# Optimization experiments

Measured on AMD Instinct MI355X. Metric: run time of the kernel, lower is better.

## Reference

```python
import jax, jax.numpy as jnp
import numpy as np

NUM_EMBEDDINGS = 512
EMBEDDING_DIM = 64
COMMITMENT_COST = 0.25
N_TOKENS = 262144


def setup_inputs() -> dict:
    key = jax.random.key(0)
    kz, kc = jax.random.split(key)
    z = jax.random.normal(kz, (N_TOKENS, EMBEDDING_DIM), dtype=jnp.float32)
    # nn.Embedding weight init: uniform(-1/num_embeddings, 1/num_embeddings)
    codebook = jax.random.uniform(
        kc, (NUM_EMBEDDINGS, EMBEDDING_DIM), dtype=jnp.float32,
        minval=-1.0 / NUM_EMBEDDINGS, maxval=1.0 / NUM_EMBEDDINGS)
    return {"z": z, "codebook": codebook}


def reference(z, codebook):
    # squared L2 distances: [N, K]
    distances = (jnp.sum(z * z, axis=1, keepdims=True)
                 + jnp.sum(codebook * codebook, axis=1)
                 - 2.0 * z @ codebook.T)
    encoding_indices = jnp.argmin(distances, axis=1)  # [N]
    z_q = codebook[encoding_indices]                  # [N, D] gather

    e_latent_loss = jnp.mean((jax.lax.stop_gradient(z_q) - z) ** 2)
    q_latent_loss = jnp.mean((z_q - jax.lax.stop_gradient(z)) ** 2)
    loss = q_latent_loss + COMMITMENT_COST * e_latent_loss

    # straight-through estimator
    z_q_st = z + jax.lax.stop_gradient(z_q - z)
    return (z_q_st, loss)
```

## Files before the change

kernel.cpp:

```cpp
#include <hip/hip_runtime.h>
#include <hip/hip_bf16.h>

#define N_TOKENS   262144
#define DIM        64
#define KCODES     512
#define OUT_ELEMS  (N_TOKENS * DIM)
#define LOSS_SCALE (1.25f / 16777216.0f)

typedef float  f32x4 __attribute__((ext_vector_type(4)));
typedef float  f32x8 __attribute__((ext_vector_type(8)));
typedef int    i32x4 __attribute__((ext_vector_type(4)));
typedef int    i32x2 __attribute__((ext_vector_type(2)));

static __device__ __forceinline__ long pack_fp8x8(const f32x8 v) {
    int lo = __builtin_amdgcn_cvt_pk_fp8_f32(v[0], v[1], 0, false);
    lo     = __builtin_amdgcn_cvt_pk_fp8_f32(v[2], v[3], lo, true);
    int hi = __builtin_amdgcn_cvt_pk_fp8_f32(v[4], v[5], 0, false);
    hi     = __builtin_amdgcn_cvt_pk_fp8_f32(v[6], v[7], hi, true);
    i32x2 r = {lo, hi};
    return __builtin_bit_cast(long, r);
}

__global__ void vq_prep(const float* __restrict__ cb,
                        unsigned char* __restrict__ cbf,
                        float* __restrict__ c2,
                        float* __restrict__ out_loss) {
    const int k = blockIdx.x;
    const int d = threadIdx.x;
    const float v = cb[k * DIM + d];
    float s = v * v;
    #pragma unroll
    for (int sh = 1; sh < 64; sh <<= 1) s += __shfl_xor(s, sh, 64);
    if (d == 0) c2[k] = 128.0f * s + 256.0f;

    const int t = k >> 4, li = k & 15;
    const int kk = d >> 5, hi = (d >> 3) & 3, j = d & 7;
    const int slot = (t * 2 + kk) * 64 + hi * 16 + li;
    const int p = __builtin_amdgcn_cvt_pk_fp8_f32(-256.0f * v, 0.0f, 0, false);
    cbf[slot * 8 + j] = (unsigned char)(p & 0xFF);

    if (k == 0 && d == 0) *out_loss = 0.0f;
}

__global__ __launch_bounds__(512, 4) void vq_main(
    const float* __restrict__ z,
    const float* __restrict__ cb,
    const unsigned char* __restrict__ cbf,
    const float* __restrict__ c2g,
    float* __restrict__ out)
{
    __shared__ unsigned char cbs[KCODES * DIM];
    __shared__ float c2s[KCODES];
    __shared__ int   keysl[8][32];
    __shared__ float lpart[8];

    const int tid  = threadIdx.x;
    const int wave = tid >> 6;
    const int lane = tid & 63;
    const int li   = lane & 15;
    const int hi   = lane >> 4;

    const int token0 = blockIdx.x * 256 + wave * 32;

    const float* zb = z + (size_t)token0 * DIM + li * DIM + hi * 8;
    const f32x8 v00 = *(const f32x8*)(zb);
    const f32x8 v01 = *(const f32x8*)(zb + 32);
    const f32x8 v10 = *(const f32x8*)(zb + 16 * DIM);
    const f32x8 v11 = *(const f32x8*)(zb + 16 * DIM + 32);

    #pragma unroll
    for (int i = 0; i < 4; ++i)
        ((i32x4*)cbs)[i * 512 + tid] = ((const i32x4*)cbf)[i * 512 + tid];
    c2s[tid] = c2g[tid];

    long af[2][2];
    float z2[2];
    {
        float zs = 0.f;
        #pragma unroll
        for (int j = 0; j < 8; ++j) zs += v00[j] * v00[j] + v01[j] * v01[j];
        af[0][0] = pack_fp8x8(v00);
        af[0][1] = pack_fp8x8(v01);
        zs += __shfl_xor(zs, 16, 64);
        zs += __shfl_xor(zs, 32, 64);
        z2[0] = zs;
    }
    {
        float zs = 0.f;
        #pragma unroll
        for (int j = 0; j < 8; ++j) zs += v10[j] * v10[j] + v11[j] * v11[j];
        af[1][0] = pack_fp8x8(v10);
        af[1][1] = pack_fp8x8(v11);
        zs += __shfl_xor(zs, 16, 64);
        zs += __shfl_xor(zs, 32, 64);
        z2[1] = zs;
    }
    __syncthreads();

    unsigned bkey[2][4];
    #pragma unroll
    for (int m = 0; m < 2; ++m)
        #pragma unroll
        for (int r = 0; r < 4; ++r) bkey[m][r] = 0xFFFFFFFFu;

    #pragma unroll 4
    for (int t = 0; t < 32; ++t) {
        const long b0 = *(const long*)&cbs[((t * 2 + 0) * 64 + lane) * 8];
        const long b1 = *(const long*)&cbs[((t * 2 + 1) * 64 + lane) * 8];
        const float cv = c2s[t * 16 + li];
        const unsigned code = (unsigned)(t * 16 + li);
        #pragma unroll
        for (int m = 0; m < 2; ++m) {
            f32x4 acc = {cv, cv, cv, cv};
            acc = __builtin_amdgcn_mfma_f32_16x16x32_fp8_fp8(af[m][0], b0, acc, 0, 0, 0);
            acc = __builtin_amdgcn_mfma_f32_16x16x32_fp8_fp8(af[m][1], b1, acc, 0, 0, 0);
            #pragma unroll
            for (int r = 0; r < 4; ++r) {
                const unsigned key = (__builtin_bit_cast(unsigned, acc[r]) & ~511u) | code;
                if (key < bkey[m][r]) bkey[m][r] = key;
            }
        }
    }

    #pragma unroll
    for (int sh = 1; sh < 16; sh <<= 1) {
        #pragma unroll
        for (int m = 0; m < 2; ++m)
            #pragma unroll
            for (int r = 0; r < 4; ++r) {
                const unsigned ok = (unsigned)__shfl_xor((int)bkey[m][r], sh, 64);
                if (ok < bkey[m][r]) bkey[m][r] = ok;
            }
    }

    if (li == 0) {
        #pragma unroll
        for (int m = 0; m < 2; ++m)
            #pragma unroll
            for (int r = 0; r < 4; ++r)
                keysl[wave][m * 16 + hi * 4 + r] = (int)bkey[m][r];
    }

    float lossp = 0.f;
    #pragma unroll
    for (int m = 0; m < 2; ++m) {
        const unsigned key = (unsigned)keysl[wave][m * 16 + li];
        const int code = (int)(key & 511u);
        if (hi == 0) {
            const float kf = __builtin_bit_cast(float, key & ~511u);
            lossp += __builtin_fmaf(kf - 256.0f, 0.0078125f, z2[m]);
        }
        const float* cbr = cb + code * DIM + hi * 8;
        const f32x8 q0 = *(const f32x8*)(cbr);
        const f32x8 q1 = *(const f32x8*)(cbr + 32);
        float* op = out + (size_t)(token0 + m * 16 + li) * DIM + hi * 8;
        *(f32x8*)(op)      = q0;
        *(f32x8*)(op + 32) = q1;
    }

    #pragma unroll
    for (int sh = 1; sh < 64; sh <<= 1) lossp += __shfl_xor(lossp, sh, 64);
    if (lane == 0) lpart[wave] = lossp;
    __syncthreads();
    if (tid == 0) {
        float s = 0.f;
        #pragma unroll
        for (int w = 0; w < 8; ++w) s += lpart[w];
        atomicAdd(out + OUT_ELEMS, s * LOSS_SCALE);
    }
}

extern "C" void kernel_launch(void* const* d_in, const int* in_sizes, int n_in,
                              void* d_out, int out_size, void* d_ws, size_t ws_size,
                              hipStream_t stream) {
    const float* z  = (const float*)d_in[0];
    const float* cb = (const float*)d_in[1];
    float* out = (float*)d_out;

    unsigned char* cbf = (unsigned char*)d_ws;
    float* c2 = (float*)((char*)d_ws + KCODES * DIM);

    vq_prep<<<KCODES, 64, 0, stream>>>(cb, cbf, c2, out + OUT_ELEMS);
    vq_main<<<N_TOKENS / 256, 512, 0, stream>>>(z, cb, cbf, c2, out);
}
```

Measured before the change: 37.80 us.

## Process two token tiles per wave with prefetch and nontemporal output stores

Blocks shrink to 256 threads (4 waves), and each wave now handles two 32-token tiles. The second tile's z loads are issued before the first tile is processed, which overlaps global loads with MFMA work. Output stores become nontemporal to avoid polluting the cache. Each block keeps the same 256 tokens and still loads the full 32KB codebook into LDS, so per-block staging is unchanged while waves per block halve. Occupancy and latency hiding may shift.

```diff
diff --git a/kernel.cpp b/kernel.cpp
--- a/kernel.cpp
+++ b/kernel.cpp
@@ -42,7 +42,7 @@
     if (k == 0 && d == 0) *out_loss = 0.0f;
 }
 
-__global__ __launch_bounds__(512, 4) void vq_main(
+__global__ __launch_bounds__(256, 4) void vq_main(
     const float* __restrict__ z,
     const float* __restrict__ cb,
     const unsigned char* __restrict__ cbf,
@@ -51,8 +51,8 @@
 {
     __shared__ unsigned char cbs[KCODES * DIM];
     __shared__ float c2s[KCODES];
-    __shared__ int   keysl[8][32];
-    __shared__ float lpart[8];
+    __shared__ int   keysl[4][32];
+    __shared__ float lpart[4];
 
     const int tid  = threadIdx.x;
     const int wave = tid >> 6;
@@ -60,112 +60,130 @@
     const int li   = lane & 15;
     const int hi   = lane >> 4;
 
-    const int token0 = blockIdx.x * 256 + wave * 32;
-
-    const float* zb = z + (size_t)token0 * DIM + li * DIM + hi * 8;
-    const f32x8 v00 = *(const f32x8*)(zb);
-    const f32x8 v01 = *(const f32x8*)(zb + 32);
-    const f32x8 v10 = *(const f32x8*)(zb + 16 * DIM);
-    const f32x8 v11 = *(const f32x8*)(zb + 16 * DIM + 32);
+    const int   tile0  = blockIdx.x * 8 + wave * 2;
+    const float* zb0 = z + (size_t)tile0 * 32 * DIM + li * DIM + hi * 8;
+
+    const f32x8 c00 = *(const f32x8*)(zb0);
+    const f32x8 c01 = *(const f32x8*)(zb0 + 32);
+    const f32x8 c10 = *(const f32x8*)(zb0 + 16 * DIM);
+    const f32x8 c11 = *(const f32x8*)(zb0 + 16 * DIM + 32);
 
     #pragma unroll
-    for (int i = 0; i < 4; ++i)
-        ((i32x4*)cbs)[i * 512 + tid] = ((const i32x4*)cbf)[i * 512 + tid];
-    c2s[tid] = c2g[tid];
-
-    long af[2][2];
-    float z2[2];
-    {
-        float zs = 0.f;
+    for (int i = 0; i < 8; ++i)
+        ((i32x4*)cbs)[i * 256 + tid] = ((const i32x4*)cbf)[i * 256 + tid];
+    c2s[tid]       = c2g[tid];
+    c2s[tid + 256] = c2g[tid + 256];
+    __syncthreads();
+
+    const float* zb1 = zb0 + 32 * DIM;
+    const f32x8 n00 = *(const f32x8*)(zb1);
+    const f32x8 n01 = *(const f32x8*)(zb1 + 32);
+    const f32x8 n10 = *(const f32x8*)(zb1 + 16 * DIM);
+    const f32x8 n11 = *(const f32x8*)(zb1 + 16 * DIM + 32);
+    __builtin_amdgcn_sched_barrier(0);
+
+    auto process = [&](const f32x8& v00, const f32x8& v01,
+                       const f32x8& v10, const f32x8& v11,
+                       int token0) -> float {
+        long af0k0, af0k1, af1k0, af1k1;
+        float z2[2];
+        {
+            float zs = 0.f;
+            #pragma unroll
+            for (int j = 0; j < 8; ++j) zs += v00[j] * v00[j] + v01[j] * v01[j];
+            af0k0 = pack_fp8x8(v00);
+            af0k1 = pack_fp8x8(v01);
+            zs += __shfl_xor(zs, 16, 64);
+            zs += __shfl_xor(zs, 32, 64);
+            z2[0] = zs;
+        }
+        {
+            float zs = 0.f;
+            #pragma unroll
+            for (int j = 0; j < 8; ++j) zs += v10[j] * v10[j] + v11[j] * v11[j];
+            af1k0 = pack_fp8x8(v10);
+            af1k1 = pack_fp8x8(v11);
+            zs += __shfl_xor(zs, 16, 64);
+            zs += __shfl_xor(zs, 32, 64);
+            z2[1] = zs;
+        }
+
+        unsigned bkey[2][4];
         #pragma unroll
-        for (int j = 0; j < 8; ++j) zs += v00[j] * v00[j] + v01[j] * v01[j];
-        af[0][0] = pack_fp8x8(v00);
-        af[0][1] = pack_fp8x8(v01);
-        zs += __shfl_xor(zs, 16, 64);
-        zs += __shfl_xor(zs, 32, 64);
-        z2[0] = zs;
-    }
-    {
-        float zs = 0.f;
+        for (int m = 0; m < 2; ++m)
+            #pragma unroll
+            for (int r = 0; r < 4; ++r) bkey[m][r] = 0xFFFFFFFFu;
+
+        #pragma unroll 4
+        for (int t = 0; t < 32; ++t) {
+            const long b0 = *(const long*)&cbs[((t * 2 + 0) * 64 + lane) * 8];
+            const long b1 = *(const long*)&cbs[((t * 2 + 1) * 64 + lane) * 8];
+            const float cv = c2s[t * 16 + li];
+            const unsigned code = (unsigned)(t * 16 + li);
+            #pragma unroll
+            for (int m = 0; m < 2; ++m) {
+                f32x4 acc = {cv, cv, cv, cv};
+                acc = __builtin_amdgcn_mfma_f32_16x16x32_fp8_fp8(
+                          m ? af1k0 : af0k0, b0, acc, 0, 0, 0);
+                acc = __builtin_amdgcn_mfma_f32_16x16x32_fp8_fp8(
+                          m ? af1k1 : af0k1, b1, acc, 0, 0, 0);
+                #pragma unroll
+                for (int r = 0; r < 4; ++r) {
+                    const unsigned key =
+                        (__builtin_bit_cast(unsigned, acc[r]) & ~511u) | code;
+                    if (key < bkey[m][r]) bkey[m][r] = key;
+                }
+            }
+        }
+
         #pragma unroll
-        for (int j = 0; j < 8; ++j) zs += v10[j] * v10[j] + v11[j] * v11[j];
-        af[1][0] = pack_fp8x8(v10);
-        af[1][1] = pack_fp8x8(v11);
-        zs += __shfl_xor(zs, 16, 64);
-        zs += __shfl_xor(zs, 32, 64);
-        z2[1] = zs;
-    }
-    __syncthreads();
-
-    unsigned bkey[2][4];
-    #pragma unroll
-    for (int m = 0; m < 2; ++m)
-        #pragma unroll
-        for (int r = 0; r < 4; ++r) bkey[m][r] = 0xFFFFFFFFu;
-
-    #pragma unroll 4
-    for (int t = 0; t < 32; ++t) {
-        const long b0 = *(const long*)&cbs[((t * 2 + 0) * 64 + lane) * 8];
-        const long b1 = *(const long*)&cbs[((t * 2 + 1) * 64 + lane) * 8];
-        const float cv = c2s[t * 16 + li];
-        const unsigned code = (unsigned)(t * 16 + li);
+        for (int sh = 1; sh < 16; sh <<= 1) {
+            #pragma unroll
+            for (int m = 0; m < 2; ++m)
+                #pragma unroll
+                for (int r = 0; r < 4; ++r) {
+                    const unsigned ok = (unsigned)__shfl_xor((int)bkey[m][r], sh, 64);
+                    if (ok < bkey[m][r]) bkey[m][r] = ok;
+                }
+        }
+
+        if (li == 0) {
+            #pragma unroll
+            for (int m = 0; m < 2; ++m)
+                #pragma unroll
+                for (int r = 0; r < 4; ++r)
+                    keysl[wave][m * 16 + hi * 4 + r] = (int)bkey[m][r];
+        }
+
+        float lp = 0.f;
         #pragma unroll
         for (int m = 0; m < 2; ++m) {
-            f32x4 acc = {cv, cv, cv, cv};
-            acc = __builtin_amdgcn_mfma_f32_16x16x32_fp8_fp8(af[m][0], b0, acc, 0, 0, 0);
-            acc = __builtin_amdgcn_mfma_f32_16x16x32_fp8_fp8(af[m][1], b1, acc, 0, 0, 0);
-            #pragma unroll
-            for (int r = 0; r < 4; ++r) {
-                const unsigned key = (__builtin_bit_cast(unsigned, acc[r]) & ~511u) | code;
-                if (key < bkey[m][r]) bkey[m][r] = key;
+            const unsigned key = (unsigned)keysl[wave][m * 16 + li];
+            const int code = (int)(key & 511u);
+            if (hi == 0) {
+                const float kf = __builtin_bit_cast(float, key & ~511u);
+                lp += __builtin_fmaf(kf - 256.0f, 0.0078125f, z2[m]);
             }
-        }
-    }
-
-    #pragma unroll
-    for (int sh = 1; sh < 16; sh <<= 1) {
-        #pragma unroll
-        for (int m = 0; m < 2; ++m)
-            #pragma unroll
-            for (int r = 0; r < 4; ++r) {
-                const unsigned ok = (unsigned)__shfl_xor((int)bkey[m][r], sh, 64);
-                if (ok < bkey[m][r]) bkey[m][r] = ok;
-            }
-    }
-
-    if (li == 0) {
-        #pragma unroll
-        for (int m = 0; m < 2; ++m)
-            #pragma unroll
-            for (int r = 0; r < 4; ++r)
-                keysl[wave][m * 16 + hi * 4 + r] = (int)bkey[m][r];
-    }
+            const float* cbr = cb + code * DIM + hi * 8;
+            const f32x8 q0 = *(const f32x8*)(cbr);
+            const f32x8 q1 = *(const f32x8*)(cbr + 32);
+            float* op = out + (size_t)(token0 + m * 16 + li) * DIM + hi * 8;
+            __builtin_nontemporal_store(q0, (f32x8*)(op));
+            __builtin_nontemporal_store(q1, (f32x8*)(op + 32));
+        }
+        return lp;
+    };
 
     float lossp = 0.f;
-    #pragma unroll
-    for (int m = 0; m < 2; ++m) {
-        const unsigned key = (unsigned)keysl[wave][m * 16 + li];
-        const int code = (int)(key & 511u);
-        if (hi == 0) {
-            const float kf = __builtin_bit_cast(float, key & ~511u);
-            lossp += __builtin_fmaf(kf - 256.0f, 0.0078125f, z2[m]);
-        }
-        const float* cbr = cb + code * DIM + hi * 8;
-        const f32x8 q0 = *(const f32x8*)(cbr);
-        const f32x8 q1 = *(const f32x8*)(cbr + 32);
-        float* op = out + (size_t)(token0 + m * 16 + li) * DIM + hi * 8;
-        *(f32x8*)(op)      = q0;
-        *(f32x8*)(op + 32) = q1;
-    }
+    lossp += process(c00, c01, c10, c11, tile0 * 32);
+    lossp += process(n00, n01, n10, n11, (tile0 + 1) * 32);
 
     #pragma unroll
     for (int sh = 1; sh < 64; sh <<= 1) lossp += __shfl_xor(lossp, sh, 64);
     if (lane == 0) lpart[wave] = lossp;
     __syncthreads();
     if (tid == 0) {
-        float s = 0.f;
-        #pragma unroll
-        for (int w = 0; w < 8; ++w) s += lpart[w];
+        const float s = lpart[0] + lpart[1] + lpart[2] + lpart[3];
         atomicAdd(out + OUT_ELEMS, s * LOSS_SCALE);
     }
 }
@@ -181,5 +199,5 @@
     float* c2 = (float*)((char*)d_ws + KCODES * DIM);
 
     vq_prep<<<KCODES, 64, 0, stream>>>(cb, cbf, c2, out + OUT_ELEMS);
-    vq_main<<<N_TOKENS / 256, 512, 0, stream>>>(z, cb, cbf, c2, out);
-}
+    vq_main<<<N_TOKENS / 256, 256, 0, stream>>>(z, cb, cbf, c2, out);
+}
```

Measured after the change: 44.12 us. +16.7%, slower.

## Split codebook gather into separate kernel with nontemporal stores

Applied to the files above, without the earlier changes.

Splits the fused kernel in two. The argmin kernel now writes only per-token keys to workspace, and a new gather kernel reads each key, fetches the codebook row and writes the output with nontemporal stores, using fully coalesced linear indexing. The goal is to remove the scattered 64 MB output write from the compute-heavy argmin kernel and let the write stream at full bandwidth. The cost is an extra kernel launch plus a round trip of the key array through memory.

```diff
diff --git a/kernel.cpp b/kernel.cpp
--- a/kernel.cpp
+++ b/kernel.cpp
@@ -42,12 +42,12 @@
     if (k == 0 && d == 0) *out_loss = 0.0f;
 }
 
-__global__ __launch_bounds__(512, 4) void vq_main(
+__global__ __launch_bounds__(512, 4) void vq_argmin(
     const float* __restrict__ z,
-    const float* __restrict__ cb,
     const unsigned char* __restrict__ cbf,
     const float* __restrict__ c2g,
-    float* __restrict__ out)
+    unsigned* __restrict__ keys,
+    float* __restrict__ out_loss)
 {
     __shared__ unsigned char cbs[KCODES * DIM];
     __shared__ float c2s[KCODES];
@@ -145,17 +145,11 @@
     #pragma unroll
     for (int m = 0; m < 2; ++m) {
         const unsigned key = (unsigned)keysl[wave][m * 16 + li];
-        const int code = (int)(key & 511u);
         if (hi == 0) {
             const float kf = __builtin_bit_cast(float, key & ~511u);
             lossp += __builtin_fmaf(kf - 256.0f, 0.0078125f, z2[m]);
+            keys[token0 + m * 16 + li] = key;
         }
-        const float* cbr = cb + code * DIM + hi * 8;
-        const f32x8 q0 = *(const f32x8*)(cbr);
-        const f32x8 q1 = *(const f32x8*)(cbr + 32);
-        float* op = out + (size_t)(token0 + m * 16 + li) * DIM + hi * 8;
-        *(f32x8*)(op)      = q0;
-        *(f32x8*)(op + 32) = q1;
     }
 
     #pragma unroll
@@ -166,7 +160,23 @@
         float s = 0.f;
         #pragma unroll
         for (int w = 0; w < 8; ++w) s += lpart[w];
-        atomicAdd(out + OUT_ELEMS, s * LOSS_SCALE);
+        atomicAdd(out_loss, s * LOSS_SCALE);
+    }
+}
+
+__global__ __launch_bounds__(256, 4) void vq_gather(
+    const float* __restrict__ cb,
+    const unsigned* __restrict__ keys,
+    float* __restrict__ out)
+{
+    const int base = blockIdx.x * 1024 + threadIdx.x;
+    #pragma unroll
+    for (int i = 0; i < 4; ++i) {
+        const int c = base + i * 256;
+        const int token = c >> 3, part = c & 7;
+        const int code = (int)(keys[token] & 511u);
+        const f32x8 q = *(const f32x8*)(cb + code * DIM + part * 8);
+        __builtin_nontemporal_store(q, (f32x8*)(out + (size_t)c * 8));
     }
 }
 
@@ -177,9 +187,11 @@
     const float* cb = (const float*)d_in[1];
     float* out = (float*)d_out;
 
-    unsigned char* cbf = (unsigned char*)d_ws;
-    float* c2 = (float*)((char*)d_ws + KCODES * DIM);
+    unsigned char* cbf  = (unsigned char*)d_ws;
+    float*         c2   = (float*)((char*)d_ws + KCODES * DIM);
+    unsigned*      keys = (unsigned*)((char*)d_ws + KCODES * DIM + KCODES * 4);
 
     vq_prep<<<KCODES, 64, 0, stream>>>(cb, cbf, c2, out + OUT_ELEMS);
-    vq_main<<<N_TOKENS / 256, 512, 0, stream>>>(z, cb, cbf, c2, out);
+    vq_argmin<<<N_TOKENS / 256, 512, 0, stream>>>(z, cbf, c2, keys, out + OUT_ELEMS);
+    vq_gather<<<(N_TOKENS * 8) / 1024, 256, 0, stream>>>(cb, keys, out);
 }
```

Measured after the change: 60.18 us. +59.2%, slower.

## Process two token tiles per wave with prefetch of the second tile

Applied to the files above, without the earlier changes.

Each block now handles 512 tokens, so each wave processes two 32-token tiles. The second tile's z loads are issued before the first tile's compute, with a sched_barrier to hold that order. This halves the grid and amortizes the per-block codebook LDS fill. Output stores become nontemporal. In exchange it raises register pressure and reduces the number of blocks, which may hurt occupancy or load balance.

```diff
diff --git a/kernel.cpp b/kernel.cpp
--- a/kernel.cpp
+++ b/kernel.cpp
@@ -42,6 +42,86 @@
     if (k == 0 && d == 0) *out_loss = 0.0f;
 }
 
+#define TILE_BODY(V00, V01, V10, V11, TOK0)                                            \
+    {                                                                                  \
+        long af00, af01, af10, af11;                                                   \
+        float z2a, z2b;                                                                \
+        {                                                                              \
+            float zs = 0.f;                                                            \
+            _Pragma("unroll")                                                          \
+            for (int j = 0; j < 8; ++j) zs += (V00)[j] * (V00)[j] + (V01)[j] * (V01)[j]; \
+            af00 = pack_fp8x8(V00); af01 = pack_fp8x8(V01);                            \
+            zs += __shfl_xor(zs, 16, 64); zs += __shfl_xor(zs, 32, 64);                \
+            z2a = zs;                                                                  \
+        }                                                                              \
+        {                                                                              \
+            float zs = 0.f;                                                            \
+            _Pragma("unroll")                                                          \
+            for (int j = 0; j < 8; ++j) zs += (V10)[j] * (V10)[j] + (V11)[j] * (V11)[j]; \
+            af10 = pack_fp8x8(V10); af11 = pack_fp8x8(V11);                            \
+            zs += __shfl_xor(zs, 16, 64); zs += __shfl_xor(zs, 32, 64);                \
+            z2b = zs;                                                                  \
+        }                                                                              \
+        unsigned bkey[2][4];                                                           \
+        _Pragma("unroll")                                                              \
+        for (int m = 0; m < 2; ++m)                                                    \
+            _Pragma("unroll")                                                          \
+            for (int r = 0; r < 4; ++r) bkey[m][r] = 0xFFFFFFFFu;                      \
+        _Pragma("unroll 4")                                                            \
+        for (int t = 0; t < 32; ++t) {                                                 \
+            const long b0 = *(const long*)&cbs[((t * 2 + 0) * 64 + lane) * 8];         \
+            const long b1 = *(const long*)&cbs[((t * 2 + 1) * 64 + lane) * 8];         \
+            const float cv = c2s[t * 16 + li];                                         \
+            const unsigned code = (unsigned)(t * 16 + li);                             \
+            _Pragma("unroll")                                                          \
+            for (int m = 0; m < 2; ++m) {                                              \
+                f32x4 acc = {cv, cv, cv, cv};                                          \
+                acc = __builtin_amdgcn_mfma_f32_16x16x32_fp8_fp8(                      \
+                          m ? af10 : af00, b0, acc, 0, 0, 0);                          \
+                acc = __builtin_amdgcn_mfma_f32_16x16x32_fp8_fp8(                      \
+                          m ? af11 : af01, b1, acc, 0, 0, 0);                          \
+                _Pragma("unroll")                                                      \
+                for (int r = 0; r < 4; ++r) {                                          \
+                    const unsigned key =                                               \
+                        (__builtin_bit_cast(unsigned, acc[r]) & ~511u) | code;         \
+                    if (key < bkey[m][r]) bkey[m][r] = key;                            \
+                }                                                                      \
+            }                                                                          \
+        }                                                                              \
+        _Pragma("unroll")                                                              \
+        for (int sh = 1; sh < 16; sh <<= 1) {                                          \
+            _Pragma("unroll")                                                          \
+            for (int m = 0; m < 2; ++m)                                                \
+                _Pragma("unroll")                                                      \
+                for (int r = 0; r < 4; ++r) {                                          \
+                    const unsigned ok = (unsigned)__shfl_xor((int)bkey[m][r], sh, 64); \
+                    if (ok < bkey[m][r]) bkey[m][r] = ok;                              \
+                }                                                                      \
+        }                                                                              \
+        if (li == 0) {                                                                 \
+            _Pragma("unroll")                                                          \
+            for (int m = 0; m < 2; ++m)                                                \
+                _Pragma("unroll")                                                      \
+                for (int r = 0; r < 4; ++r)                                            \
+                    keysl[wave][m * 16 + hi * 4 + r] = (int)bkey[m][r];                \
+        }                                                                              \
+        _Pragma("unroll")                                                              \
+        for (int m = 0; m < 2; ++m) {                                                  \
+            const unsigned key = (unsigned)keysl[wave][m * 16 + li];                   \
+            const int code = (int)(key & 511u);                                        \
+            if (hi == 0) {                                                             \
+                const float kf = __builtin_bit_cast(float, key & ~511u);               \
+                lossp += __builtin_fmaf(kf - 256.0f, 0.0078125f, m ? z2b : z2a);       \
+            }                                                                          \
+            const float* cbr = cb + code * DIM + hi * 8;                               \
+            const f32x8 q0 = *(const f32x8*)(cbr);                                     \
+            const f32x8 q1 = *(const f32x8*)(cbr + 32);                                \
+            float* op = out + (size_t)((TOK0) + m * 16 + li) * DIM + hi * 8;           \
+            __builtin_nontemporal_store(q0, (f32x8*)(op));                             \
+            __builtin_nontemporal_store(q1, (f32x8*)(op + 32));                        \
+        }                                                                              \
+    }
+
 __global__ __launch_bounds__(512, 4) void vq_main(
     const float* __restrict__ z,
     const float* __restrict__ cb,
@@ -60,103 +140,30 @@
     const int li   = lane & 15;
     const int hi   = lane >> 4;
 
-    const int token0 = blockIdx.x * 256 + wave * 32;
+    const int token0 = blockIdx.x * 512 + wave * 64;
 
-    const float* zb = z + (size_t)token0 * DIM + li * DIM + hi * 8;
-    const f32x8 v00 = *(const f32x8*)(zb);
-    const f32x8 v01 = *(const f32x8*)(zb + 32);
-    const f32x8 v10 = *(const f32x8*)(zb + 16 * DIM);
-    const f32x8 v11 = *(const f32x8*)(zb + 16 * DIM + 32);
+    const float* zb0 = z + (size_t)token0 * DIM + li * DIM + hi * 8;
+    const f32x8 c00 = *(const f32x8*)(zb0);
+    const f32x8 c01 = *(const f32x8*)(zb0 + 32);
+    const f32x8 c10 = *(const f32x8*)(zb0 + 16 * DIM);
+    const f32x8 c11 = *(const f32x8*)(zb0 + 16 * DIM + 32);
 
     #pragma unroll
     for (int i = 0; i < 4; ++i)
         ((i32x4*)cbs)[i * 512 + tid] = ((const i32x4*)cbf)[i * 512 + tid];
     c2s[tid] = c2g[tid];
-
-    long af[2][2];
-    float z2[2];
-    {
-        float zs = 0.f;
-        #pragma unroll
-        for (int j = 0; j < 8; ++j) zs += v00[j] * v00[j] + v01[j] * v01[j];
-        af[0][0] = pack_fp8x8(v00);
-        af[0][1] = pack_fp8x8(v01);
-        zs += __shfl_xor(zs, 16, 64);
-        zs += __shfl_xor(zs, 32, 64);
-        z2[0] = zs;
-    }
-    {
-        float zs = 0.f;
-        #pragma unroll
-        for (int j = 0; j < 8; ++j) zs += v10[j] * v10[j] + v11[j] * v11[j];
-        af[1][0] = pack_fp8x8(v10);
-        af[1][1] = pack_fp8x8(v11);
-        zs += __shfl_xor(zs, 16, 64);
-        zs += __shfl_xor(zs, 32, 64);
-        z2[1] = zs;
-    }
     __syncthreads();
 
-    unsigned bkey[2][4];
-    #pragma unroll
-    for (int m = 0; m < 2; ++m)
-        #pragma unroll
-        for (int r = 0; r < 4; ++r) bkey[m][r] = 0xFFFFFFFFu;
-
-    #pragma unroll 4
-    for (int t = 0; t < 32; ++t) {
-        const long b0 = *(const long*)&cbs[((t * 2 + 0) * 64 + lane) * 8];
-        const long b1 = *(const long*)&cbs[((t * 2 + 1) * 64 + lane) * 8];
-        const float cv = c2s[t * 16 + li];
-        const unsigned code = (unsigned)(t * 16 + li);
-        #pragma unroll
-        for (int m = 0; m < 2; ++m) {
-            f32x4 acc = {cv, cv, cv, cv};
-            acc = __builtin_amdgcn_mfma_f32_16x16x32_fp8_fp8(af[m][0], b0, acc, 0, 0, 0);
-            acc = __builtin_amdgcn_mfma_f32_16x16x32_fp8_fp8(af[m][1], b1, acc, 0, 0, 0);
-            #pragma unroll
-            for (int r = 0; r < 4; ++r) {
-                const unsigned key = (__builtin_bit_cast(unsigned, acc[r]) & ~511u) | code;
-                if (key < bkey[m][r]) bkey[m][r] = key;
-            }
-        }
-    }
-
-    #pragma unroll
-    for (int sh = 1; sh < 16; sh <<= 1) {
-        #pragma unroll
-        for (int m = 0; m < 2; ++m)
-            #pragma unroll
-            for (int r = 0; r < 4; ++r) {
-                const unsigned ok = (unsigned)__shfl_xor((int)bkey[m][r], sh, 64);
-                if (ok < bkey[m][r]) bkey[m][r] = ok;
-            }
-    }
-
-    if (li == 0) {
-        #pragma unroll
-        for (int m = 0; m < 2; ++m)
-            #pragma unroll
-            for (int r = 0; r < 4; ++r)
-                keysl[wave][m * 16 + hi * 4 + r] = (int)bkey[m][r];
-    }
+    const float* zb1 = zb0 + 32 * DIM;
+    const f32x8 n00 = *(const f32x8*)(zb1);
+    const f32x8 n01 = *(const f32x8*)(zb1 + 32);
+    const f32x8 n10 = *(const f32x8*)(zb1 + 16 * DIM);
+    const f32x8 n11 = *(const f32x8*)(zb1 + 16 * DIM + 32);
+    __builtin_amdgcn_sched_barrier(0);
 
     float lossp = 0.f;
-    #pragma unroll
-    for (int m = 0; m < 2; ++m) {
-        const unsigned key = (unsigned)keysl[wave][m * 16 + li];
-        const int code = (int)(key & 511u);
-        if (hi == 0) {
-            const float kf = __builtin_bit_cast(float, key & ~511u);
-            lossp += __builtin_fmaf(kf - 256.0f, 0.0078125f, z2[m]);
-        }
-        const float* cbr = cb + code * DIM + hi * 8;
-        const f32x8 q0 = *(const f32x8*)(cbr);
-        const f32x8 q1 = *(const f32x8*)(cbr + 32);
-        float* op = out + (size_t)(token0 + m * 16 + li) * DIM + hi * 8;
-        *(f32x8*)(op)      = q0;
-        *(f32x8*)(op + 32) = q1;
-    }
+    TILE_BODY(c00, c01, c10, c11, token0);
+    TILE_BODY(n00, n01, n10, n11, token0 + 32);
 
     #pragma unroll
     for (int sh = 1; sh < 64; sh <<= 1) lossp += __shfl_xor(lossp, sh, 64);
@@ -181,5 +188,5 @@
     float* c2 = (float*)((char*)d_ws + KCODES * DIM);
 
     vq_prep<<<KCODES, 64, 0, stream>>>(cb, cbf, c2, out + OUT_ELEMS);
-    vq_main<<<N_TOKENS / 256, 512, 0, stream>>>(z, cb, cbf, c2, out);
+    vq_main<<<N_TOKENS / 512, 512, 0, stream>>>(z, cb, cbf, c2, out);
 }
```

After: 46.57 us. 23.2% more time.
